# Kernel tuning notes

Hardware: AMD Instinct MI355X
Metric: run time of the kernel (lower is better)

Reference implementation:

```python
import jax, jax.numpy as jnp
import numpy as np

N = 32768        # num_nodes
D = 256          # hidden_dim
H = 8            # num_heads
DH = D // H      # head_dim
S = 4            # num_scales
CS = max(3, N // 10)          # cluster size (pos=None path)
C = (N + CS - 1) // CS        # num_clusters
EPS = 1e-5


def setup_inputs() -> dict:
    key = jax.random.key(0)
    ks = jax.random.split(key, 16)
    w = 0.02
    return {
        "x": jax.random.normal(ks[0], (N, D), dtype=jnp.float32),
        "edge_index": jax.random.randint(ks[1], (2, 16 * N), 0, N),
        "batch": jnp.zeros((N,), dtype=jnp.int32),
        # per-scale AttentionPooling params (stacked over S)
        "Wk": jax.random.normal(ks[2], (S, D, D), dtype=jnp.float32) * w,
        "bk": jnp.zeros((S, D), dtype=jnp.float32),
        "Wv": jax.random.normal(ks[3], (S, D, D), dtype=jnp.float32) * w,
        "bv": jnp.zeros((S, D), dtype=jnp.float32),
        "Wo": jax.random.normal(ks[4], (S, D, D), dtype=jnp.float32) * w,
        "bo": jnp.zeros((S, D), dtype=jnp.float32),
        "pool_query": jax.random.normal(ks[5], (S, H, DH), dtype=jnp.float32),
        # scale fusion params
        "Wf1": jax.random.normal(ks[6], (S * D, D), dtype=jnp.float32) * w,
        "bf1": jnp.zeros((D,), dtype=jnp.float32),
        "ln_g": jnp.ones((D,), dtype=jnp.float32),
        "ln_b": jnp.zeros((D,), dtype=jnp.float32),
        "Wf2": jax.random.normal(ks[7], (D, D), dtype=jnp.float32) * w,
        "bf2": jnp.zeros((D,), dtype=jnp.float32),
    }


def reference(x, edge_index, batch, Wk, bk, Wv, bv, Wo, bo, pool_query,
              Wf1, bf1, ln_g, ln_b, Wf2, bf2):
    # clusters from pos=None branch: arange(N) // cluster_size (same at all scales)
    clusters = jnp.arange(N) // CS                                  # [N]
    scale = DH ** -0.5

    # all S scales vectorized (params stacked on axis s)
    keys = (jnp.einsum('nd,sde->nse', x, Wk) + bk).reshape(N, S, H, DH)
    values = (jnp.einsum('nd,sde->nse', x, Wv) + bv).reshape(N, S, H, DH)

    # pool_query is identical for every node -> scores[n,s,h] = <k, q> * scale
    scores = jnp.einsum('nshd,shd->nsh', keys, pool_query) * scale  # [N,S,H]

    # per-cluster softmax over the node dim (segment softmax)
    smax = jax.ops.segment_max(scores, clusters, num_segments=C)    # [C,S,H]
    ex = jnp.exp(scores - smax[clusters])
    denom = jax.ops.segment_sum(ex, clusters, num_segments=C)
    weights = ex / denom[clusters]                                  # [N,S,H]

    # attended values, scatter-mean over clusters
    attended = (weights[..., None] * values).reshape(N, S, D)       # [N,S,D]
    counts = jax.ops.segment_sum(jnp.ones((N,), dtype=x.dtype), clusters, num_segments=C)
    pooled = jax.ops.segment_sum(attended, clusters, num_segments=C) / counts[:, None, None]

    # out_proj then gather back to nodes
    out = jnp.einsum('csd,sde->cse', pooled, Wo) + bo               # [C,S,D]
    node = out[clusters]                                            # [N,S,D]

    # scale fusion: Linear -> LayerNorm -> GELU -> (Dropout eval=id) -> Linear
    combined = node.reshape(N, S * D)
    h = combined @ Wf1 + bf1
    mu = jnp.mean(h, axis=-1, keepdims=True)
    var = jnp.mean(jnp.square(h - mu), axis=-1, keepdims=True)
    h = (h - mu) / jnp.sqrt(var + EPS) * ln_g + ln_b
    h = jax.nn.gelu(h, approximate=False)
    fused = h @ Wf2 + bf2                                           # [N,D]
    return fused
```

## Files before the change

### kernel.cpp

```cpp
#include <hip/hip_runtime.h>
#include <math.h>


namespace {
constexpr int N   = 32768;
constexpr int CS  = 3276;
constexpr int CPC = 52;
constexpr int NB  = CPC*10 + 1;

constexpr size_t CQ_OFF   = 0;
constexpr size_t WQBF_OFF = 32;
constexpr size_t PART_OFF = WQBF_OFF + 4096;
constexpr size_t PS_OFF   = PART_OFF + (size_t)NB*8192;
constexpr size_t XW_OFF   = PS_OFF + 352;
constexpr size_t PL_OFF   = XW_OFF + 90112;
constexpr size_t OL_OFF   = PL_OFF + 11264;
constexpr size_t HP_OFF   = OL_OFF + 11264;
constexpr size_t FP_OFF   = HP_OFF + 11264;
}

typedef __attribute__((ext_vector_type(8))) short short8;
typedef __attribute__((ext_vector_type(4))) float f32x4;

__device__ __forceinline__ unsigned f2bf(float f){
  unsigned u = __float_as_uint(f);
  unsigned r = u + 0x7FFFu + ((u >> 16) & 1u);
  return r >> 16;
}

__global__ __launch_bounds__(256) void ka(const float* __restrict__ Wk, const float* __restrict__ bk,
                                          const float* __restrict__ pq, float* __restrict__ ws){
  int b = blockIdx.x, t = threadIdx.x;
  const float scale = 0.17677669529663688f;
  if (b < 32){
    __shared__ float row[256];
    int s = b >> 3, h = b & 7;
    const float* wrow = Wk + ((size_t)s<<16) + (size_t)t*256 + h*32;
    const float* q = pq + (s*8 + h)*32;
    float a = 0.f;
#pragma unroll
    for (int j=0;j<32;j++) a = fmaf(wrow[j], q[j], a);
    row[t] = a*scale;
    __syncthreads();
    if (t < 32){
      int ks = t & 7, kg2 = t >> 3;
      const float* src = row + ks*32 + kg2*8;
      uint4 p;
      p.x = f2bf(src[0]) | (f2bf(src[1]) << 16);
      p.y = f2bf(src[2]) | (f2bf(src[3]) << 16);
      p.z = f2bf(src[4]) | (f2bf(src[5]) << 16);
      p.w = f2bf(src[6]) | (f2bf(src[7]) << 16);
      int Nt = b >> 4, l15b = b & 15;
      ((uint4*)(ws + WQBF_OFF))[(size_t)(Nt*8 + ks)*64 + l15b + 16*kg2] = p;
    }
  } else {
    if (t < 32){
      int s = t >> 3, h = t & 7;
      const float* br = bk + s*256 + h*32;
      const float* q = pq + t*32;
      float a = 0.f;
#pragma unroll
      for (int j=0;j<32;j++) a = fmaf(br[j], q[j], a);
      ws[CQ_OFF + t] = a*scale;
    }
    for (int i = t; i < 352; i += 256) ws[PS_OFF + i] = 0.f;
  }
}

__global__ __launch_bounds__(512,4) void kbd9(const float* __restrict__ x, float* __restrict__ ws){
  int b = blockIdx.x, t = threadIdx.x;
  int c  = (b < 520) ? (b / CPC) : 10;
  int wi = (b < 520) ? (b % CPC) : 0;
  int n0 = c*CS + wi*64;
  int n1 = min(n0 + 64, min((c+1)*CS, N));
  int cnt = n1 - n0;

  __shared__ unsigned short xtb[64*264];
  __shared__ float sw[64*36];
  __shared__ float psb[16*32];

  int wv = t >> 6, lane = t & 63;
  int Mt = wv & 3, Nt = wv >> 2;
  int l15 = lane & 15, kg = lane >> 4;
  int arow = Mt*16 + l15;
  uint4 bfr[8];
  const uint4* WQBF4 = (const uint4*)(ws + WQBF_OFF);
#pragma unroll
  for (int ks=0; ks<8; ++ks) bfr[ks] = WQBF4[(size_t)(Nt*8 + ks)*64 + lane];
  float cqv = ws[CQ_OFF + Nt*16 + l15];
  int shc = Nt*16 + l15;

  const float4* X4 = (const float4*)x;
#pragma unroll
  for (int k=0;k<8;k++){
    int f = t + k*512;
    int j = f >> 6, c4 = f & 63;
    if (n0 + j < N){
      float4 v = X4[(size_t)(n0+j)*64 + c4];
      uint2 p;
      p.x = f2bf(v.x) | (f2bf(v.y) << 16);
      p.y = f2bf(v.z) | (f2bf(v.w) << 16);
      *(uint2*)(xtb + j*264 + c4*4) = p;
    }
  }
  __syncthreads();

  f32x4 acc1 = {0.f, 0.f, 0.f, 0.f};
#pragma unroll
  for (int ks=0; ks<8; ++ks){
    union { uint4 q; short8 v; } A, B;
    A.q = *(const uint4*)(xtb + arow*264 + ks*32 + kg*8);
    B.q = bfr[ks];
    acc1 = __builtin_amdgcn_mfma_f32_16x16x32_bf16(A.v, B.v, acc1, 0, 0, 0);
  }
  float s4 = 0.f;
#pragma unroll
  for (int r=0;r<4;r++){
    int jl = Mt*16 + kg*4 + r;
    float e = __expf(acc1[r] + cqv);
    sw[jl*36 + shc] = e;
    if (jl < cnt) s4 += e;
  }
  psb[(Mt*4 + kg)*32 + shc] = s4;
  __syncthreads();
  if (t < 32){
    float S = 0.f;
#pragma unroll
    for (int k=0;k<16;k++) S += psb[k*32 + t];
    unsafeAtomicAdd(ws + PS_OFF + (size_t)c*32 + t, S);
  }

  int shq = t >> 6, dq = t & 63;
  float acc[16];
#pragma unroll
  for (int q=0;q<16;q++) acc[q] = 0.f;
#pragma unroll 4
  for (int j=0;j<cnt;++j){
    uint2 u = *(const uint2*)(xtb + j*264 + dq*4);
    float x0 = __uint_as_float(u.x << 16);
    float x1 = __uint_as_float(u.x & 0xffff0000u);
    float x2 = __uint_as_float(u.y << 16);
    float x3 = __uint_as_float(u.y & 0xffff0000u);
    float4 wv2 = *(const float4*)(sw + j*36 + shq*4);
    acc[0]  = fmaf(wv2.x, x0, acc[0]);  acc[1]  = fmaf(wv2.x, x1, acc[1]);
    acc[2]  = fmaf(wv2.x, x2, acc[2]);  acc[3]  = fmaf(wv2.x, x3, acc[3]);
    acc[4]  = fmaf(wv2.y, x0, acc[4]);  acc[5]  = fmaf(wv2.y, x1, acc[5]);
    acc[6]  = fmaf(wv2.y, x2, acc[6]);  acc[7]  = fmaf(wv2.y, x3, acc[7]);
    acc[8]  = fmaf(wv2.z, x0, acc[8]);  acc[9]  = fmaf(wv2.z, x1, acc[9]);
    acc[10] = fmaf(wv2.z, x2, acc[10]); acc[11] = fmaf(wv2.z, x3, acc[11]);
    acc[12] = fmaf(wv2.w, x0, acc[12]); acc[13] = fmaf(wv2.w, x1, acc[13]);
    acc[14] = fmaf(wv2.w, x2, acc[14]); acc[15] = fmaf(wv2.w, x3, acc[15]);
  }
  float* pr = ws + PART_OFF + (size_t)b*8192;
#pragma unroll
  for (int i=0;i<4;i++)
    *(float4*)(pr + (size_t)(shq*4+i)*256 + dq*4) =
      make_float4(acc[i*4], acc[i*4+1], acc[i*4+2], acc[i*4+3]);
}

__global__ __launch_bounds__(256) void ke2(float* __restrict__ ws){
  int b = blockIdx.x, t = threadIdx.x;
  int c = b >> 5, sh = b & 31;
  int nch = (c < 10) ? CPC : 1;
  int cb  = (c < 10) ? c*CPC : 520;
  float rden = 1.0f / ws[PS_OFF + (size_t)c*32 + sh];
  const float* part = ws + PART_OFF + (size_t)sh*256 + t;
  float a = 0.f;
  for (int k=0;k<nch;k++) a += part[(size_t)(cb+k)*8192];
  ws[XW_OFF + (size_t)c*8192 + (size_t)sh*256 + t] = a * rden;
}

__global__ __launch_bounds__(256) void kp(float* __restrict__ ws,
    const float* __restrict__ Wv, const float* __restrict__ bv){
  int b = blockIdx.x; int c = b >> 4, rem = b & 15, s = rem >> 2, eq = rem & 3;
  int t = threadIdx.x, e64 = t & 63, dq = t >> 6;
  int e = eq*64 + e64, h = e >> 5;
  const float* xr = ws + XW_OFF + (size_t)c*8192 + (size_t)(s*8 + h)*256 + dq*64;
  const float* wv = Wv + (size_t)s*65536 + (size_t)(dq*64)*256 + e;
  float a = 0.f;
#pragma unroll 8
  for (int d=0; d<64; ++d) a = fmaf(wv[(size_t)d*256], xr[d], a);
  __shared__ float red[4][64];
  red[dq][e64] = a;
  __syncthreads();
  if (t < 64){
    float rcnt = (c < 10) ? (1.0f/(float)CS) : 0.125f;
    float p = (red[0][t]+red[1][t]+red[2][t]+red[3][t] + bv[s*256 + eq*64 + t]) * rcnt;
    ws[PL_OFF + (size_t)c*1024 + s*256 + eq*64 + t] = p;
  }
}

__global__ __launch_bounds__(256) void ko(float* __restrict__ ws,
    const float* __restrict__ Wo, const float* __restrict__ bo){
  int b = blockIdx.x; int c = b >> 4, rem = b & 15, s = rem >> 2, eq = rem & 3;
  int t = threadIdx.x, e64 = t & 63, dq = t >> 6;
  int e = eq*64 + e64;
  const float* pr = ws + PL_OFF + (size_t)c*1024 + s*256 + dq*64;
  const float* wo = Wo + (size_t)s*65536 + (size_t)(dq*64)*256 + e;
  float a = 0.f;
#pragma unroll 8
  for (int d=0; d<64; ++d) a = fmaf(wo[(size_t)d*256], pr[d], a);
  __shared__ float red[4][64];
  red[dq][e64] = a;
  __syncthreads();
  if (t < 64)
    ws[OL_OFF + (size_t)c*1024 + s*256 + eq*64 + t] =
      red[0][t]+red[1][t]+red[2][t]+red[3][t] + bo[s*256 + eq*64 + t];
}

__global__ __launch_bounds__(256) void kf1(const float* __restrict__ Wf1, float* __restrict__ ws){
  int b = blockIdx.x; int c = b >> 4, fq = (b >> 2) & 3, kq = b & 3;
  int t = threadIdx.x, f64 = t & 63, ks = t >> 6;
  const float* ol = ws + OL_OFF + (size_t)c*1024 + kq*256 + ks*64;
  const float* wf = Wf1 + (size_t)(kq*256 + ks*64)*256 + fq*64 + f64;
  float a = 0.f;
#pragma unroll 8
  for (int i=0; i<64; ++i) a = fmaf(wf[(size_t)i*256], ol[i], a);
  __shared__ float red[4][64];
  red[ks][f64] = a;
  __syncthreads();
  if (t < 64)
    ws[HP_OFF + (size_t)(c*4 + kq)*256 + fq*64 + t] = red[0][t]+red[1][t]+red[2][t]+red[3][t];
}

__global__ __launch_bounds__(256) void kf2b(const float* __restrict__ Wf2, float* __restrict__ ws,
    const float* __restrict__ bf1, const float* __restrict__ lng, const float* __restrict__ lnb){
  int b = blockIdx.x; int c = b >> 4, gq = (b >> 2) & 3, kq = b & 3;
  int t = threadIdx.x;
  __shared__ float hl[256];
  __shared__ float rs1[4], rs2[4];
  float hacc = bf1[t];
#pragma unroll
  for (int q=0;q<4;q++) hacc += ws[HP_OFF + (size_t)(c*4+q)*256 + t];
  float s1 = hacc, s2v = hacc*hacc;
  for (int off=32; off>0; off>>=1){ s1 += __shfl_down(s1, off, 64); s2v += __shfl_down(s2v, off, 64); }
  int wid = t>>6, lane = t&63;
  if (lane==0){ rs1[wid]=s1; rs2[wid]=s2v; }
  __syncthreads();
  float S1 = rs1[0]+rs1[1]+rs1[2]+rs1[3];
  float S2 = rs2[0]+rs2[1]+rs2[2]+rs2[3];
  float mu = S1*(1.0f/256.0f);
  float var = S2*(1.0f/256.0f) - mu*mu;
  float rsig = rsqrtf(var + 1e-5f);
  float hn = (hacc - mu)*rsig*lng[t] + lnb[t];
  hl[t] = 0.5f*hn*(1.0f + erff(hn*0.70710678118654752f));
  __syncthreads();
  int g64 = t & 63, ks = t >> 6;
  const float* hh = hl + kq*64 + ks*16;
  const float* wf = Wf2 + (size_t)(kq*64 + ks*16)*256 + gq*64 + g64;
  float a = 0.f;
#pragma unroll
  for (int i=0; i<16; ++i) a = fmaf(wf[(size_t)i*256], hh[i], a);
  __shared__ float red[4][64];
  red[ks][g64] = a;
  __syncthreads();
  if (t < 64)
    ws[FP_OFF + (size_t)(c*4 + kq)*256 + gq*64 + t] = red[0][t]+red[1][t]+red[2][t]+red[3][t];
}

__global__ __launch_bounds__(256) void kbc2(const float* __restrict__ ws, float4* __restrict__ out,
                                            const float* __restrict__ bf2){
  unsigned bidx = blockIdx.x, t = threadIdx.x;
  unsigned idx = bidx*256u + t;
  unsigned c = (bidx*4u) / (unsigned)CS;
  __shared__ float4 row[64];
  if (t < 64){
    const float4* FP4 = (const float4*)(ws + FP_OFF);
    float4 s0 = FP4[(c*4+0)*64 + t];
    float4 s1 = FP4[(c*4+1)*64 + t];
    float4 s2 = FP4[(c*4+2)*64 + t];
    float4 s3 = FP4[(c*4+3)*64 + t];
    float4 bb = ((const float4*)bf2)[t];
    row[t] = make_float4(s0.x+s1.x+s2.x+s3.x+bb.x, s0.y+s1.y+s2.y+s3.y+bb.y,
                         s0.z+s1.z+s2.z+s3.z+bb.z, s0.w+s1.w+s2.w+s3.w+bb.w);
  }
  __syncthreads();
  out[idx] = row[t & 63u];
}

extern "C" void kernel_launch(void* const* d_in, const int* in_sizes, int n_in,
                              void* d_out, int out_size, void* d_ws, size_t ws_size,
                              hipStream_t stream) {
  const float* x   = (const float*)d_in[0];
  const float* Wk  = (const float*)d_in[3];
  const float* bk  = (const float*)d_in[4];
  const float* Wv  = (const float*)d_in[5];
  const float* bv  = (const float*)d_in[6];
  const float* Wo  = (const float*)d_in[7];
  const float* bo  = (const float*)d_in[8];
  const float* pq  = (const float*)d_in[9];
  const float* Wf1 = (const float*)d_in[10];
  const float* bf1 = (const float*)d_in[11];
  const float* lng = (const float*)d_in[12];
  const float* lnb = (const float*)d_in[13];
  const float* Wf2 = (const float*)d_in[14];
  const float* bf2 = (const float*)d_in[15];
  float* ws = (float*)d_ws;
  float4* out = (float4*)d_out;

  hipLaunchKernelGGL(ka,   dim3(33),   dim3(256), 0, stream, Wk, bk, pq, ws);
  hipLaunchKernelGGL(kbd9, dim3(NB),   dim3(512), 0, stream, x, ws);
  hipLaunchKernelGGL(ke2,  dim3(352),  dim3(256), 0, stream, ws);
  hipLaunchKernelGGL(kp,   dim3(176),  dim3(256), 0, stream, ws, Wv, bv);
  hipLaunchKernelGGL(ko,   dim3(176),  dim3(256), 0, stream, ws, Wo, bo);
  hipLaunchKernelGGL(kf1,  dim3(176),  dim3(256), 0, stream, Wf1, ws);
  hipLaunchKernelGGL(kf2b, dim3(176),  dim3(256), 0, stream, Wf2, ws, bf1, lng, lnb);
  hipLaunchKernelGGL(kbc2, dim3(8192), dim3(256), 0, stream, ws, out, bf2);
}
```

Measured before the change: 69.43 us.

## Compute weighted cluster partial sums with bf16 MFMA and transposed LDS reads

The per-chunk weighted sum of x (exp-scores times x over 64 nodes) moves from a scalar FMA loop to 16x16x32 bf16 MFMA instructions. The exp weights are stored transposed in LDS as bf16, and the x tile is read with ds_read_b64_tr_b16 to form B fragments. Out-of-range rows are zero-filled so the MFMA can always cover all 64 rows. This cuts VALU work in the main streaming kernel, at the cost of bf16 rounding of the softmax weights and scattered scalar stores of the partials.

```diff
diff --git a/kernel.cpp b/kernel.cpp
--- a/kernel.cpp
+++ b/kernel.cpp
@@ -67,7 +67,7 @@
   }
 }
 
-__global__ __launch_bounds__(512,4) void kbd9(const float* __restrict__ x, float* __restrict__ ws){
+__global__ __launch_bounds__(512,4) void kbd10(const float* __restrict__ x, float* __restrict__ ws){
   int b = blockIdx.x, t = threadIdx.x;
   int c  = (b < 520) ? (b / CPC) : 10;
   int wi = (b < 520) ? (b % CPC) : 0;
@@ -75,8 +75,8 @@
   int n1 = min(n0 + 64, min((c+1)*CS, N));
   int cnt = n1 - n0;
 
-  __shared__ unsigned short xtb[64*264];
-  __shared__ float sw[64*36];
+  __shared__ __align__(16) unsigned short xtb[64*264];
+  __shared__ __align__(16) unsigned short swT[32*72];
   __shared__ float psb[16*32];
 
   int wv = t >> 6, lane = t & 63;
@@ -95,13 +95,11 @@
   for (int k=0;k<8;k++){
     int f = t + k*512;
     int j = f >> 6, c4 = f & 63;
-    if (n0 + j < N){
-      float4 v = X4[(size_t)(n0+j)*64 + c4];
-      uint2 p;
-      p.x = f2bf(v.x) | (f2bf(v.y) << 16);
-      p.y = f2bf(v.z) | (f2bf(v.w) << 16);
-      *(uint2*)(xtb + j*264 + c4*4) = p;
-    }
+    float4 v = (n0 + j < N) ? X4[(size_t)(n0+j)*64 + c4] : make_float4(0.f,0.f,0.f,0.f);
+    uint2 p;
+    p.x = f2bf(v.x) | (f2bf(v.y) << 16);
+    p.y = f2bf(v.z) | (f2bf(v.w) << 16);
+    *(uint2*)(xtb + j*264 + c4*4) = p;
   }
   __syncthreads();
 
@@ -113,15 +111,21 @@
     B.q = bfr[ks];
     acc1 = __builtin_amdgcn_mfma_f32_16x16x32_bf16(A.v, B.v, acc1, 0, 0, 0);
   }
-  float s4 = 0.f;
-#pragma unroll
-  for (int r=0;r<4;r++){
-    int jl = Mt*16 + kg*4 + r;
-    float e = __expf(acc1[r] + cqv);
-    sw[jl*36 + shc] = e;
-    if (jl < cnt) s4 += e;
-  }
-  psb[(Mt*4 + kg)*32 + shc] = s4;
+  {
+    float ev[4];
+    float s4 = 0.f;
+#pragma unroll
+    for (int r=0;r<4;r++){
+      int jl = Mt*16 + kg*4 + r;
+      float e = (jl < cnt) ? __expf(acc1[r] + cqv) : 0.f;
+      ev[r] = e; s4 += e;
+    }
+    uint2 wp;
+    wp.x = f2bf(ev[0]) | (f2bf(ev[1]) << 16);
+    wp.y = f2bf(ev[2]) | (f2bf(ev[3]) << 16);
+    *(uint2*)(swT + (size_t)shc*72 + Mt*16 + kg*4) = wp;
+    psb[(Mt*4 + kg)*32 + shc] = s4;
+  }
   __syncthreads();
   if (t < 32){
     float S = 0.f;
@@ -130,32 +134,47 @@
     unsafeAtomicAdd(ws + PS_OFF + (size_t)c*32 + t, S);
   }
 
-  int shq = t >> 6, dq = t & 63;
-  float acc[16];
-#pragma unroll
-  for (int q=0;q<16;q++) acc[q] = 0.f;
-#pragma unroll 4
-  for (int j=0;j<cnt;++j){
-    uint2 u = *(const uint2*)(xtb + j*264 + dq*4);
-    float x0 = __uint_as_float(u.x << 16);
-    float x1 = __uint_as_float(u.x & 0xffff0000u);
-    float x2 = __uint_as_float(u.y << 16);
-    float x3 = __uint_as_float(u.y & 0xffff0000u);
-    float4 wv2 = *(const float4*)(sw + j*36 + shq*4);
-    acc[0]  = fmaf(wv2.x, x0, acc[0]);  acc[1]  = fmaf(wv2.x, x1, acc[1]);
-    acc[2]  = fmaf(wv2.x, x2, acc[2]);  acc[3]  = fmaf(wv2.x, x3, acc[3]);
-    acc[4]  = fmaf(wv2.y, x0, acc[4]);  acc[5]  = fmaf(wv2.y, x1, acc[5]);
-    acc[6]  = fmaf(wv2.y, x2, acc[6]);  acc[7]  = fmaf(wv2.y, x3, acc[7]);
-    acc[8]  = fmaf(wv2.z, x0, acc[8]);  acc[9]  = fmaf(wv2.z, x1, acc[9]);
-    acc[10] = fmaf(wv2.z, x2, acc[10]); acc[11] = fmaf(wv2.z, x3, acc[11]);
-    acc[12] = fmaf(wv2.w, x0, acc[12]); acc[13] = fmaf(wv2.w, x1, acc[13]);
-    acc[14] = fmaf(wv2.w, x2, acc[14]); acc[15] = fmaf(wv2.w, x3, acc[15]);
+  int Mt2 = wv & 1, Nq = wv >> 1;
+  union FR { uint4 q; short8 v; };
+  FR a0, a1;
+  a0.q = *(const uint4*)(swT + (size_t)(Mt2*16 + l15)*72 + kg*8);
+  a1.q = *(const uint4*)(swT + (size_t)(Mt2*16 + l15)*72 + 32 + kg*8);
+  unsigned xb = (unsigned)(size_t)&xtb[0];
+  unsigned va = xb + (unsigned)(kg*4224 + (l15>>2)*528 + (l15&3)*8 + Nq*128);
+  unsigned long long tr[4][2][2];
+#pragma unroll
+  for (int i=0;i<4;i++){
+#pragma unroll
+    for (int k2=0;k2<2;k2++){
+      asm volatile("ds_read_b64_tr_b16 %0, %2 offset:%c3\n\t"
+                   "ds_read_b64_tr_b16 %1, %2 offset:%c4"
+                   : "=v"(tr[i][k2][0]), "=v"(tr[i][k2][1])
+                   : "v"(va), "i"(i*32 + k2*16896), "i"(i*32 + k2*16896 + 2112));
+    }
+  }
+  asm volatile("s_waitcnt lgkmcnt(0)" ::: "memory");
+  __builtin_amdgcn_sched_barrier(0);
+  f32x4 o[4] = {{0.f,0.f,0.f,0.f},{0.f,0.f,0.f,0.f},{0.f,0.f,0.f,0.f},{0.f,0.f,0.f,0.f}};
+#pragma unroll
+  for (int i=0;i<4;i++){
+#pragma unroll
+    for (int k2=0;k2<2;k2++){
+      FR Bf;
+      Bf.q.x = (unsigned)(tr[i][k2][0] & 0xffffffffULL);
+      Bf.q.y = (unsigned)(tr[i][k2][0] >> 32);
+      Bf.q.z = (unsigned)(tr[i][k2][1] & 0xffffffffULL);
+      Bf.q.w = (unsigned)(tr[i][k2][1] >> 32);
+      o[i] = __builtin_amdgcn_mfma_f32_16x16x32_bf16(k2 ? a1.v : a0.v, Bf.v, o[i], 0, 0, 0);
+    }
   }
   float* pr = ws + PART_OFF + (size_t)b*8192;
 #pragma unroll
-  for (int i=0;i<4;i++)
-    *(float4*)(pr + (size_t)(shq*4+i)*256 + dq*4) =
-      make_float4(acc[i*4], acc[i*4+1], acc[i*4+2], acc[i*4+3]);
+  for (int i=0;i<4;i++){
+    int dcol = Nq*64 + i*16 + l15;
+#pragma unroll
+    for (int r=0;r<4;r++)
+      pr[(size_t)(Mt2*16 + kg*4 + r)*256 + dcol] = o[i][r];
+  }
 }
 
 __global__ __launch_bounds__(256) void ke2(float* __restrict__ ws){
@@ -298,12 +317,12 @@
   float* ws = (float*)d_ws;
   float4* out = (float4*)d_out;
 
-  hipLaunchKernelGGL(ka,   dim3(33),   dim3(256), 0, stream, Wk, bk, pq, ws);
-  hipLaunchKernelGGL(kbd9, dim3(NB),   dim3(512), 0, stream, x, ws);
-  hipLaunchKernelGGL(ke2,  dim3(352),  dim3(256), 0, stream, ws);
-  hipLaunchKernelGGL(kp,   dim3(176),  dim3(256), 0, stream, ws, Wv, bv);
-  hipLaunchKernelGGL(ko,   dim3(176),  dim3(256), 0, stream, ws, Wo, bo);
-  hipLaunchKernelGGL(kf1,  dim3(176),  dim3(256), 0, stream, Wf1, ws);
-  hipLaunchKernelGGL(kf2b, dim3(176),  dim3(256), 0, stream, Wf2, ws, bf1, lng, lnb);
-  hipLaunchKernelGGL(kbc2, dim3(8192), dim3(256), 0, stream, ws, out, bf2);
-}
+  hipLaunchKernelGGL(ka,    dim3(33),   dim3(256), 0, stream, Wk, bk, pq, ws);
+  hipLaunchKernelGGL(kbd10, dim3(NB),   dim3(512), 0, stream, x, ws);
+  hipLaunchKernelGGL(ke2,   dim3(352),  dim3(256), 0, stream, ws);
+  hipLaunchKernelGGL(kp,    dim3(176),  dim3(256), 0, stream, ws, Wv, bv);
+  hipLaunchKernelGGL(ko,    dim3(176),  dim3(256), 0, stream, ws, Wo, bo);
+  hipLaunchKernelGGL(kf1,   dim3(176),  dim3(256), 0, stream, Wf1, ws);
+  hipLaunchKernelGGL(kf2b,  dim3(176),  dim3(256), 0, stream, Wf2, ws, bf1, lng, lnb);
+  hipLaunchKernelGGL(kbc2,  dim3(8192), dim3(256), 0, stream, ws, out, bf2);
+}
```

Measured after the change: 61.76 us. -11.0%, faster.
